# Kernel optimization log

Measured on AMD Instinct MI355X. Metric: run time of the kernel, lower is better.

## Reference

```python
import jax, jax.numpy as jnp
import numpy as np

N_NODES = 51200
N_GRAPHS = 64
NODES_PER_GRAPH = 800
N_EDGES = 819200
DIM_IN = 128
DIM_HIDDEN = 64
HEADS = 3
DIM_OUT = 64


def leaky(x, slope):
    return jnp.where(x >= 0, x, slope * x)


def setup_inputs() -> dict:
    key = jax.random.key(0)
    ks = jax.random.split(key, 12)
    s = lambda fan_in: 1.0 / np.sqrt(fan_in)
    X = jax.random.normal(ks[0], (N_NODES, DIM_IN), dtype=jnp.float32)
    edge_indices = jax.random.randint(ks[1], (2, N_EDGES), 0, N_NODES, dtype=jnp.int32)
    ptr = (jnp.arange(N_GRAPHS + 1, dtype=jnp.int32) * NODES_PER_GRAPH)
    # linearSeq: Linear(dim_in, dim_hidden) + LeakyReLU
    W1 = jax.random.uniform(ks[2], (DIM_IN, DIM_HIDDEN), jnp.float32, -s(DIM_IN), s(DIM_IN))
    b1 = jax.random.uniform(ks[3], (DIM_HIDDEN,), jnp.float32, -s(DIM_IN), s(DIM_IN))
    # GATConv params: lin_src/lin_dst (no bias), att_src/att_dst, bias (concat=False -> out_channels)
    W_src = jax.random.uniform(ks[4], (DIM_HIDDEN, HEADS * DIM_HIDDEN), jnp.float32, -s(DIM_HIDDEN), s(DIM_HIDDEN))
    W_dst = jax.random.uniform(ks[5], (DIM_HIDDEN, HEADS * DIM_HIDDEN), jnp.float32, -s(DIM_HIDDEN), s(DIM_HIDDEN))
    att_src = jax.random.normal(ks[6], (HEADS, DIM_HIDDEN), dtype=jnp.float32) * 0.1
    att_dst = jax.random.normal(ks[7], (HEADS, DIM_HIDDEN), dtype=jnp.float32) * 0.1
    gat_bias = jnp.zeros((DIM_HIDDEN,), dtype=jnp.float32)
    # linear_final: Linear(2*dim_hidden, dim_out)
    Wf = jax.random.uniform(ks[8], (2 * DIM_HIDDEN, DIM_OUT), jnp.float32, -s(2 * DIM_HIDDEN), s(2 * DIM_HIDDEN))
    bf = jax.random.uniform(ks[9], (DIM_OUT,), jnp.float32, -s(2 * DIM_HIDDEN), s(2 * DIM_HIDDEN))
    return {"X": X, "W1": W1, "b1": b1, "W_src": W_src, "W_dst": W_dst,
            "att_src": att_src, "att_dst": att_dst, "gat_bias": gat_bias,
            "Wf": Wf, "bf": bf, "edge_indices": edge_indices, "ptr": ptr}


def reference(X, W1, b1, W_src, W_dst, att_src, att_dst, gat_bias, Wf, bf, edge_indices, ptr):
    N = X.shape[0]
    src, dst = edge_indices[0], edge_indices[1]  # message flows src -> dst
    # input projection
    h = leaky(X @ W1 + b1, 0.01)                                  # [N, DH]
    # GATConv (heads=3, concat=False, add_self_loops=False)
    x_src = (h @ W_src).reshape(N, HEADS, DIM_HIDDEN)             # [N, H, C]
    x_dst = (h @ W_dst).reshape(N, HEADS, DIM_HIDDEN)
    a_src = jnp.einsum('nhc,hc->nh', x_src, att_src)              # [N, H]
    a_dst = jnp.einsum('nhc,hc->nh', x_dst, att_dst)
    logits = leaky(a_src[src] + a_dst[dst], 0.2)                  # [E, H]
    # segment softmax over incoming edges of each target node
    m = jax.ops.segment_max(logits, dst, num_segments=N)          # [N, H]
    e = jnp.exp(logits - m[dst])
    denom = jax.ops.segment_sum(e, dst, num_segments=N)           # [N, H]
    attn = e / denom[dst]                                         # [E, H]
    msg = x_src[src] * attn[..., None]                            # [E, H, C]
    agg = jax.ops.segment_sum(msg, dst, num_segments=N)           # [N, H, C]
    out = agg.mean(axis=1) + gat_bias                             # concat=False -> head mean
    # final head
    cat = jnp.concatenate([h, out], axis=1)                       # [N, 2*DH]
    y = leaky(cat, 0.01) @ Wf + bf                                # [N, DO]
    # aggregate_using_ptr: mean-pool nodes per graph using CSR ptr
    node_graph = jnp.searchsorted(ptr, jnp.arange(N), side='right') - 1
    sums = jax.ops.segment_sum(y, node_graph, num_segments=ptr.shape[0] - 1)
    counts = (ptr[1:] - ptr[:-1]).astype(y.dtype)
    pooled = sums / counts[:, None]                               # [n_graphs, DO]
    return pooled, attn
```

## Files before the change

### kernel.cpp

```cpp
#include <hip/hip_runtime.h>
#include <hip/hip_bf16.h>

#define N_NODES   51200
#define N_GRAPHS  64
#define N_EDGES   819200
#define DIM_IN    128
#define DH        64
#define HEADS     3
#define DIM_OUT   64
#define CAP       96
#define NPART     8
#define PART_SZ   (N_NODES / NPART)

typedef __hip_bfloat16 bf16;
typedef short bf16x8 __attribute__((ext_vector_type(8)));
typedef float f32x4  __attribute__((ext_vector_type(4)));
typedef float f32x2  __attribute__((ext_vector_type(2)));

__device__ __forceinline__ float b2f(bf16 x) { return __bfloat162float(x); }
__device__ __forceinline__ bf16  f2b(float x) { return __float2bfloat16(x); }
__device__ __forceinline__ short f2bs(float x) { return (short)__bfloat16_as_ushort(f2b(x)); }
__device__ __forceinline__ float leaky(float x, float s) { return x >= 0.f ? x : s * x; }
__device__ __forceinline__ float ldin(const void* p, size_t i, int f32) {
    return f32 ? ((const float*)p)[i] : b2f(((const bf16*)p)[i]);
}
__device__ __forceinline__ bf16x8 ld8(const void* p, size_t i, int f32) {
    if (!f32) return *((const bf16x8*)((const short*)p + i));
    const float* f = (const float*)p + i;
    bf16x8 r;
    #pragma unroll
    for (int j = 0; j < 8; ++j) r[j] = f2bs(f[j]);
    return r;
}

__global__ __launch_bounds__(256) void detect_kernel(const unsigned short* __restrict__ Xu,
                                                     int* __restrict__ flag) {
    __shared__ int cnt;
    int tid = threadIdx.x;
    if (tid == 0) cnt = 0;
    __syncthreads();
    int local = 0;
    for (int i = tid * 2; i < 8192; i += 512) {
        unsigned e = (Xu[i] >> 7) & 0xFF;
        if (e >= 110 && e <= 135) local++;
    }
    atomicAdd(&cnt, local);
    __syncthreads();
    if (tid == 0) *flag = (cnt < 2048) ? 1 : 0;
}

__global__ __launch_bounds__(256) void scatter_prep_kernel(const int* __restrict__ src,
                                                           const int* __restrict__ dst,
                                                           int* __restrict__ cursor,
                                                           unsigned short* __restrict__ bucket,
                                                           const void* __restrict__ W1,
                                                           const void* __restrict__ Wsrc,
                                                           const void* __restrict__ Wdst,
                                                           const void* __restrict__ Wf,
                                                           const void* __restrict__ att_src,
                                                           const void* __restrict__ att_dst,
                                                           const int* __restrict__ flagp,
                                                           short* __restrict__ W1t,
                                                           short* __restrict__ Wallt,
                                                           short* __restrict__ Wft,
                                                           short* __restrict__ Wat) {
    if (blockIdx.x < NPART * (N_EDGES / 2048)) {
        const int p = blockIdx.x & (NPART - 1);
        const int slice = blockIdx.x >> 3;
        const int lo = p * PART_SZ, hi = lo + PART_SZ;
        const int base = slice * 2048 + threadIdx.x;
        #pragma unroll
        for (int t = 0; t < 8; ++t) {
            int e = base + t * 256;
            int d = dst[e];
            if (d >= lo && d < hi) {
                int pos = atomicAdd(&cursor[d], 1);
                if (pos < CAP) bucket[(size_t)d * CAP + pos] = (unsigned short)src[e];
            }
        }
        return;
    }
    const int f32 = *flagp;
    int idx = (blockIdx.x - NPART * (N_EDGES / 2048)) * 256 + threadIdx.x;
    if (idx < 8192) {
        int n = idx >> 7, k = idx & 127;
        W1t[idx] = f2bs(ldin(W1, (size_t)k * 64 + n, f32));
    } else if (idx < 8192 + 12288) {
        int j = idx - 8192;
        int n = j >> 6, k = j & 63;
        Wallt[j] = f2bs(ldin(Wsrc, (size_t)k * 192 + n, f32));
    } else if (idx < 8192 + 12288 + 8192) {
        int j = idx - 20480;
        int n = j >> 7, k = j & 127;
        Wft[j] = f2bs(ldin(Wf, (size_t)k * 64 + n, f32));
    } else if (idx < 8192 + 12288 + 8192 + 1024) {
        int j = idx - 28672;
        int n = j >> 6, k = j & 63;
        float v = 0.f;
        if (n < 3) {
            for (int c = 0; c < 64; ++c)
                v += ldin(Wsrc, (size_t)k * 192 + n * 64 + c, f32) * ldin(att_src, n * 64 + c, f32);
        } else if (n < 6) {
            for (int c = 0; c < 64; ++c)
                v += ldin(Wdst, (size_t)k * 192 + (n - 3) * 64 + c, f32) * ldin(att_dst, (n - 3) * 64 + c, f32);
        }
        Wat[j] = f2bs(v);
    }
}

__global__ __launch_bounds__(256) void k1_kernel(const void* __restrict__ X,
                                                 const short* __restrict__ W1t,
                                                 const short* __restrict__ Wallt,
                                                 const short* __restrict__ Wat,
                                                 const void* __restrict__ b1,
                                                 const int* __restrict__ flagp,
                                                 bf16* __restrict__ h_bf,
                                                 unsigned* __restrict__ x8,
                                                 float* __restrict__ a_src4,
                                                 float* __restrict__ a_dst4) {
    const int f32 = *flagp;
    __shared__ short hs[64 * 72];
    const int tid  = threadIdx.x;
    const int w    = tid >> 6;
    const int lane = tid & 63;
    const int lm   = lane & 15;
    const int q    = lane >> 4;
    const int row0 = blockIdx.x * 64;

    const float bias = ldin(b1, w * 16 + lm, f32);
    for (int mt = 0; mt < 4; ++mt) {
        f32x4 acc = {0.f, 0.f, 0.f, 0.f};
        #pragma unroll
        for (int kc = 0; kc < 4; ++kc) {
            bf16x8 a = ld8(X, (size_t)(row0 + mt * 16 + lm) * 128 + kc * 32 + q * 8, f32);
            bf16x8 b = *((const bf16x8*)(W1t + (size_t)(w * 16 + lm) * 128 + kc * 32 + q * 8));
            acc = __builtin_amdgcn_mfma_f32_16x16x32_bf16(a, b, acc, 0, 0, 0);
        }
        #pragma unroll
        for (int r = 0; r < 4; ++r) {
            int row = mt * 16 + q * 4 + r;
            float v = leaky(acc[r] + bias, 0.01f);
            short hv = f2bs(v);
            hs[row * 72 + w * 16 + lm] = hv;
            h_bf[(size_t)(row0 + row) * 64 + w * 16 + lm] = __ushort_as_bfloat16((unsigned short)hv);
        }
    }
    __syncthreads();

    for (int mt = 0; mt < 4; ++mt) {
        bf16x8 a0 = *((const bf16x8*)(hs + (mt * 16 + lm) * 72 + q * 8));
        bf16x8 a1 = *((const bf16x8*)(hs + (mt * 16 + lm) * 72 + 32 + q * 8));
        f32x4 acc[3];
        #pragma unroll
        for (int hh = 0; hh < 3; ++hh) {
            acc[hh] = (f32x4){0.f, 0.f, 0.f, 0.f};
            bf16x8 b0 = *((const bf16x8*)(Wallt + (size_t)(hh * 64 + w * 16 + lm) * 64 + q * 8));
            bf16x8 b1v = *((const bf16x8*)(Wallt + (size_t)(hh * 64 + w * 16 + lm) * 64 + 32 + q * 8));
            acc[hh] = __builtin_amdgcn_mfma_f32_16x16x32_bf16(a0, b0, acc[hh], 0, 0, 0);
            acc[hh] = __builtin_amdgcn_mfma_f32_16x16x32_bf16(a1, b1v, acc[hh], 0, 0, 0);
        }
        #pragma unroll
        for (int r = 0; r < 4; ++r) {
            int row = row0 + mt * 16 + q * 4 + r;
            unsigned p = (unsigned)__builtin_amdgcn_cvt_pk_fp8_f32(acc[0][r], acc[1][r], 0, false);
            p = (unsigned)__builtin_amdgcn_cvt_pk_fp8_f32(acc[2][r], 0.f, (int)p, true);
            x8[(size_t)row * 64 + w * 16 + lm] = p;
        }
        if (w == mt) {
            f32x4 acca = {0.f, 0.f, 0.f, 0.f};
            bf16x8 b0 = *((const bf16x8*)(Wat + (size_t)lm * 64 + q * 8));
            bf16x8 b1v = *((const bf16x8*)(Wat + (size_t)lm * 64 + 32 + q * 8));
            acca = __builtin_amdgcn_mfma_f32_16x16x32_bf16(a0, b0, acca, 0, 0, 0);
            acca = __builtin_amdgcn_mfma_f32_16x16x32_bf16(a1, b1v, acca, 0, 0, 0);
            if (lm < 6) {
                #pragma unroll
                for (int r = 0; r < 4; ++r) {
                    int row = row0 + mt * 16 + q * 4 + r;
                    if (lm < 3) a_src4[(size_t)row * 4 + lm] = acca[r];
                    else        a_dst4[(size_t)row * 4 + (lm - 3)] = acca[r];
                }
            }
        }
    }
}

__global__ __launch_bounds__(256) void edge_kernel(const unsigned short* __restrict__ bucket,
                                                   const int* __restrict__ cursor,
                                                   const float* __restrict__ a_src4,
                                                   const float* __restrict__ a_dst4,
                                                   const unsigned* __restrict__ x8,
                                                   const void* __restrict__ gat_bias,
                                                   const int* __restrict__ flagp,
                                                   float4* __restrict__ dstinfo,
                                                   bf16* __restrict__ out_agg) {
    const int f32 = *flagp;
    const int lane = threadIdx.x & 63;
    const int w = threadIdx.x >> 6;
    const int n = blockIdx.x * 4 + w;
    const int dg = min(cursor[n], CAP);
    const float4 ad = ((const float4*)a_dst4)[n];
    __shared__ float4 buf[4][64];
    float den0 = 0.f, den1 = 0.f, den2 = 0.f;
    float acc0 = 0.f, acc1 = 0.f, acc2 = 0.f;
    for (int c0 = 0; c0 < dg; c0 += 64) {
        int cnt = min(64, dg - c0);
        if (lane < cnt) {
            int s = bucket[(size_t)n * CAP + c0 + lane];
            const float4 as = ((const float4*)a_src4)[s];
            float e0 = __expf(leaky(as.x + ad.x, 0.2f));
            float e1 = __expf(leaky(as.y + ad.y, 0.2f));
            float e2 = __expf(leaky(as.z + ad.z, 0.2f));
            buf[w][lane] = make_float4(e0, e1, e2, __int_as_float(s));
        }
        asm volatile("s_waitcnt lgkmcnt(0)" ::: "memory");
        int j = 0;
        for (; j + 8 <= cnt; j += 8) {
            float4 r[8]; int xv[8];
            #pragma unroll
            for (int u = 0; u < 8; ++u) r[u] = buf[w][j + u];
            #pragma unroll
            for (int u = 0; u < 8; ++u)
                xv[u] = (int)x8[(size_t)__float_as_int(r[u].w) * 64 + lane];
            #pragma unroll
            for (int u = 0; u < 8; ++u) {
                f32x2 p = __builtin_amdgcn_cvt_pk_f32_fp8(xv[u], false);
                acc0 += r[u].x * p[0];
                acc1 += r[u].y * p[1];
                acc2 += r[u].z * __builtin_amdgcn_cvt_f32_fp8(xv[u], 2);
                den0 += r[u].x; den1 += r[u].y; den2 += r[u].z;
            }
        }
        for (; j < cnt; ++j) {
            float4 r = buf[w][j];
            int xv = (int)x8[(size_t)__float_as_int(r.w) * 64 + lane];
            f32x2 p = __builtin_amdgcn_cvt_pk_f32_fp8(xv, false);
            acc0 += r.x * p[0];
            acc1 += r.y * p[1];
            acc2 += r.z * __builtin_amdgcn_cvt_f32_fp8(xv, 2);
            den0 += r.x; den1 += r.y; den2 += r.z;
        }
    }
    float inv0 = den0 > 0.f ? 1.f / den0 : 0.f;
    float inv1 = den1 > 0.f ? 1.f / den1 : 0.f;
    float inv2 = den2 > 0.f ? 1.f / den2 : 0.f;
    float outv = (acc0 * inv0 + acc1 * inv1 + acc2 * inv2) * (1.f / 3.f) + ldin(gat_bias, lane, f32);
    out_agg[(size_t)n * DH + lane] = f2b(outv);
    if (lane == 0) {
        dstinfo[(size_t)n * 2 + 0] = make_float4(ad.x, ad.y, ad.z, 0.f);
        dstinfo[(size_t)n * 2 + 1] = make_float4(inv0, inv1, inv2, 0.f);
    }
}

__global__ __launch_bounds__(256) void attn_g3_kernel(const int* __restrict__ src,
                                                      const int* __restrict__ dst,
                                                      const float* __restrict__ a_src4,
                                                      const float4* __restrict__ dstinfo,
                                                      const bf16* __restrict__ h_bf,
                                                      const bf16* __restrict__ out_agg,
                                                      const short* __restrict__ Wft,
                                                      const void* __restrict__ bfv,
                                                      const int* __restrict__ flagp,
                                                      bf16* __restrict__ y_bf,
                                                      void* __restrict__ d_out) {
    const int f32 = *flagp;
    __shared__ short cs[64 * 136];
    if (blockIdx.x < N_EDGES / 256) {
        int e = blockIdx.x * 256 + threadIdx.x;
        int s = src[e], d = dst[e];
        const float4 as = ((const float4*)a_src4)[s];
        const float4 ad = dstinfo[(size_t)d * 2 + 0];
        const float4 cv = dstinfo[(size_t)d * 2 + 1];
        float a0 = __expf(leaky(as.x + ad.x, 0.2f)) * cv.x;
        float a1 = __expf(leaky(as.y + ad.y, 0.2f)) * cv.y;
        float a2 = __expf(leaky(as.z + ad.z, 0.2f)) * cv.z;
        size_t o = (size_t)N_GRAPHS * DIM_OUT + (size_t)e * 3;
        if (f32) {
            float* p = (float*)d_out;
            p[o] = a0; p[o + 1] = a1; p[o + 2] = a2;
        } else {
            bf16* p = (bf16*)d_out;
            p[o] = f2b(a0); p[o + 1] = f2b(a1); p[o + 2] = f2b(a2);
        }
        return;
    }
    const int bid  = blockIdx.x - N_EDGES / 256;
    const int tid  = threadIdx.x;
    const int w    = tid >> 6;
    const int lane = tid & 63;
    const int lm   = lane & 15;
    const int q    = lane >> 4;
    const int row0 = bid * 64;
    for (int idx = tid; idx < 64 * 64; idx += 256) {
        int r = idx >> 6, k = idx & 63;
        cs[r * 136 + k] = f2bs(leaky(b2f(h_bf[(size_t)(row0 + r) * 64 + k]), 0.01f));
    }
    for (int idx = tid; idx < 64 * 64; idx += 256) {
        int r = idx >> 6, k = idx & 63;
        cs[r * 136 + 64 + k] = f2bs(leaky(b2f(out_agg[(size_t)(row0 + r) * 64 + k]), 0.01f));
    }
    __syncthreads();
    const float bias = ldin(bfv, w * 16 + lm, f32);
    for (int mt = 0; mt < 4; ++mt) {
        f32x4 acc = {0.f, 0.f, 0.f, 0.f};
        #pragma unroll
        for (int kc = 0; kc < 4; ++kc) {
            bf16x8 a = *((const bf16x8*)(cs + (mt * 16 + lm) * 136 + kc * 32 + q * 8));
            bf16x8 b = *((const bf16x8*)(Wft + (size_t)(w * 16 + lm) * 128 + kc * 32 + q * 8));
            acc = __builtin_amdgcn_mfma_f32_16x16x32_bf16(a, b, acc, 0, 0, 0);
        }
        #pragma unroll
        for (int r = 0; r < 4; ++r) {
            int row = row0 + mt * 16 + q * 4 + r;
            y_bf[(size_t)row * 64 + w * 16 + lm] = f2b(acc[r] + bias);
        }
    }
}

__global__ __launch_bounds__(1024) void pool_kernel(const bf16* __restrict__ y_bf,
                                                    const int* __restrict__ ptr,
                                                    const int* __restrict__ flagp,
                                                    void* __restrict__ d_out) {
    __shared__ float part[16][64];
    const int f32 = *flagp;
    const int g = blockIdx.x;
    const int w = threadIdx.x >> 6, lane = threadIdx.x & 63;
    const int lo = ptr[g], hi = ptr[g + 1];
    const int cnt = hi - lo;
    float s = 0.f;
    for (int i = lo + w; i < hi; i += 16) s += b2f(y_bf[(size_t)i * DIM_OUT + lane]);
    part[w][lane] = s;
    __syncthreads();
    if (threadIdx.x < 64) {
        float t = 0.f;
        #pragma unroll
        for (int k = 0; k < 16; ++k) t += part[k][threadIdx.x];
        float v = t / (float)cnt;
        if (f32) ((float*)d_out)[g * DIM_OUT + threadIdx.x] = v;
        else     ((bf16*)d_out)[g * DIM_OUT + threadIdx.x]  = f2b(v);
    }
}

extern "C" void kernel_launch(void* const* d_in, const int* in_sizes, int n_in,
                              void* d_out, int out_size, void* d_ws, size_t ws_size,
                              hipStream_t stream) {
    const void* X        = d_in[0];
    const void* W1       = d_in[1];
    const void* b1       = d_in[2];
    const void* Wsrc     = d_in[3];
    const void* Wdst     = d_in[4];
    const void* att_src  = d_in[5];
    const void* att_dst  = d_in[6];
    const void* gat_bias = d_in[7];
    const void* Wf       = d_in[8];
    const void* bfv      = d_in[9];
    const int*  ei       = (const int*)d_in[10];
    const int*  ptr      = (const int*)d_in[11];
    const int*  src  = ei;
    const int*  dstp = ei + N_EDGES;

    char* ws = (char*)d_ws;
    size_t off_b = 0;
    auto alloc = [&](size_t bytes) -> char* {
        char* p = ws + off_b;
        off_b += (bytes + 255) & ~(size_t)255;
        return p;
    };
    int*     flag    = (int*)    alloc(256);
    short*   W1t     = (short*)  alloc(8192 * 2);
    short*   Wallt   = (short*)  alloc(12288 * 2);
    short*   Wft     = (short*)  alloc(8192 * 2);
    short*   Wat     = (short*)  alloc(1024 * 2);
    bf16*    h_bf    = (bf16*)   alloc((size_t)N_NODES * 64 * 2);
    unsigned* x8     = (unsigned*)alloc((size_t)N_NODES * 64 * 4);
    float*   a_src4  = (float*)  alloc((size_t)N_NODES * 16);
    float*   a_dst4  = (float*)  alloc((size_t)N_NODES * 16);
    float4*  dstinfo = (float4*) alloc((size_t)N_NODES * 2 * 16);
    bf16*    out_agg = (bf16*)   alloc((size_t)N_NODES * 64 * 2);
    int*     cursor  = (int*)    alloc((size_t)N_NODES * 4);
    unsigned short* bucket = (unsigned short*)alloc((size_t)N_NODES * CAP * 2);
    bf16*    y_bf    = (bf16*)   x8;
    if (off_b > ws_size) return;

    hipLaunchKernelGGL(detect_kernel, dim3(1), dim3(256), 0, stream,
                       (const unsigned short*)X, flag);
    hipMemsetAsync(cursor, 0, (size_t)N_NODES * 4, stream);
    hipLaunchKernelGGL(scatter_prep_kernel,
                       dim3(NPART * (N_EDGES / 2048) + 116), dim3(256), 0, stream,
                       src, dstp, cursor, bucket,
                       W1, Wsrc, Wdst, Wf, att_src, att_dst, flag, W1t, Wallt, Wft, Wat);
    hipLaunchKernelGGL(k1_kernel, dim3(N_NODES / 64), dim3(256), 0, stream,
                       X, W1t, Wallt, Wat, b1, flag, h_bf, x8, a_src4, a_dst4);
    hipLaunchKernelGGL(edge_kernel, dim3(N_NODES / 4), dim3(256), 0, stream,
                       bucket, cursor, a_src4, a_dst4, x8, gat_bias, flag, dstinfo, out_agg);
    hipLaunchKernelGGL(attn_g3_kernel, dim3(N_EDGES / 256 + N_NODES / 64), dim3(256), 0, stream,
                       src, dstp, a_src4, dstinfo, h_bf, out_agg, Wft, bfv, flag, y_bf, d_out);
    hipLaunchKernelGGL(pool_kernel, dim3(N_GRAPHS), dim3(1024), 0, stream, y_bf, ptr, flag, d_out);
}
```

Baseline: 239.6 us.

## Aggregate h before W_src projection and apply projection after aggregation

```diff
diff --git a/kernel.cpp b/kernel.cpp
--- a/kernel.cpp
+++ b/kernel.cpp
@@ -15,7 +15,6 @@
 typedef __hip_bfloat16 bf16;
 typedef short bf16x8 __attribute__((ext_vector_type(8)));
 typedef float f32x4  __attribute__((ext_vector_type(4)));
-typedef float f32x2  __attribute__((ext_vector_type(2)));
 
 __device__ __forceinline__ float b2f(bf16 x) { return __bfloat162float(x); }
 __device__ __forceinline__ bf16  f2b(float x) { return __float2bfloat16(x); }
@@ -61,7 +60,7 @@
                                                            const void* __restrict__ att_dst,
                                                            const int* __restrict__ flagp,
                                                            short* __restrict__ W1t,
-                                                           short* __restrict__ Wallt,
+                                                           short* __restrict__ Wspt,
                                                            short* __restrict__ Wft,
                                                            short* __restrict__ Wat) {
     if (blockIdx.x < NPART * (N_EDGES / 2048)) {
@@ -85,15 +84,17 @@
     if (idx < 8192) {
         int n = idx >> 7, k = idx & 127;
         W1t[idx] = f2bs(ldin(W1, (size_t)k * 64 + n, f32));
-    } else if (idx < 8192 + 12288) {
+    } else if (idx < 20480) {
         int j = idx - 8192;
-        int n = j >> 6, k = j & 63;
-        Wallt[j] = f2bs(ldin(Wsrc, (size_t)k * 192 + n, f32));
-    } else if (idx < 8192 + 12288 + 8192) {
+        int col = j / 192;
+        int rem = j - col * 192;
+        int h = rem >> 6, kk = rem & 63;
+        Wspt[j] = f2bs(ldin(Wsrc, (size_t)kk * 192 + h * 64 + col, f32) * (1.0f / 3.0f));
+    } else if (idx < 28672) {
         int j = idx - 20480;
         int n = j >> 7, k = j & 127;
         Wft[j] = f2bs(ldin(Wf, (size_t)k * 64 + n, f32));
-    } else if (idx < 8192 + 12288 + 8192 + 1024) {
+    } else if (idx < 29696) {
         int j = idx - 28672;
         int n = j >> 6, k = j & 63;
         float v = 0.f;
@@ -110,12 +111,10 @@
 
 __global__ __launch_bounds__(256) void k1_kernel(const void* __restrict__ X,
                                                  const short* __restrict__ W1t,
-                                                 const short* __restrict__ Wallt,
                                                  const short* __restrict__ Wat,
                                                  const void* __restrict__ b1,
                                                  const int* __restrict__ flagp,
                                                  bf16* __restrict__ h_bf,
-                                                 unsigned* __restrict__ x8,
                                                  float* __restrict__ a_src4,
                                                  float* __restrict__ a_dst4) {
     const int f32 = *flagp;
@@ -147,38 +146,21 @@
     }
     __syncthreads();
 
-    for (int mt = 0; mt < 4; ++mt) {
-        bf16x8 a0 = *((const bf16x8*)(hs + (mt * 16 + lm) * 72 + q * 8));
-        bf16x8 a1 = *((const bf16x8*)(hs + (mt * 16 + lm) * 72 + 32 + q * 8));
-        f32x4 acc[3];
-        #pragma unroll
-        for (int hh = 0; hh < 3; ++hh) {
-            acc[hh] = (f32x4){0.f, 0.f, 0.f, 0.f};
-            bf16x8 b0 = *((const bf16x8*)(Wallt + (size_t)(hh * 64 + w * 16 + lm) * 64 + q * 8));
-            bf16x8 b1v = *((const bf16x8*)(Wallt + (size_t)(hh * 64 + w * 16 + lm) * 64 + 32 + q * 8));
-            acc[hh] = __builtin_amdgcn_mfma_f32_16x16x32_bf16(a0, b0, acc[hh], 0, 0, 0);
-            acc[hh] = __builtin_amdgcn_mfma_f32_16x16x32_bf16(a1, b1v, acc[hh], 0, 0, 0);
-        }
-        #pragma unroll
-        for (int r = 0; r < 4; ++r) {
-            int row = row0 + mt * 16 + q * 4 + r;
-            unsigned p = (unsigned)__builtin_amdgcn_cvt_pk_fp8_f32(acc[0][r], acc[1][r], 0, false);
-            p = (unsigned)__builtin_amdgcn_cvt_pk_fp8_f32(acc[2][r], 0.f, (int)p, true);
-            x8[(size_t)row * 64 + w * 16 + lm] = p;
-        }
-        if (w == mt) {
-            f32x4 acca = {0.f, 0.f, 0.f, 0.f};
-            bf16x8 b0 = *((const bf16x8*)(Wat + (size_t)lm * 64 + q * 8));
-            bf16x8 b1v = *((const bf16x8*)(Wat + (size_t)lm * 64 + 32 + q * 8));
-            acca = __builtin_amdgcn_mfma_f32_16x16x32_bf16(a0, b0, acca, 0, 0, 0);
-            acca = __builtin_amdgcn_mfma_f32_16x16x32_bf16(a1, b1v, acca, 0, 0, 0);
-            if (lm < 6) {
-                #pragma unroll
-                for (int r = 0; r < 4; ++r) {
-                    int row = row0 + mt * 16 + q * 4 + r;
-                    if (lm < 3) a_src4[(size_t)row * 4 + lm] = acca[r];
-                    else        a_dst4[(size_t)row * 4 + (lm - 3)] = acca[r];
-                }
+    {
+        const int mt = w;
+        bf16x8 a0  = *((const bf16x8*)(hs + (mt * 16 + lm) * 72 + q * 8));
+        bf16x8 a1  = *((const bf16x8*)(hs + (mt * 16 + lm) * 72 + 32 + q * 8));
+        bf16x8 b0  = *((const bf16x8*)(Wat + (size_t)lm * 64 + q * 8));
+        bf16x8 b1v = *((const bf16x8*)(Wat + (size_t)lm * 64 + 32 + q * 8));
+        f32x4 acca = {0.f, 0.f, 0.f, 0.f};
+        acca = __builtin_amdgcn_mfma_f32_16x16x32_bf16(a0, b0, acca, 0, 0, 0);
+        acca = __builtin_amdgcn_mfma_f32_16x16x32_bf16(a1, b1v, acca, 0, 0, 0);
+        if (lm < 6) {
+            #pragma unroll
+            for (int r = 0; r < 4; ++r) {
+                int row = row0 + mt * 16 + q * 4 + r;
+                if (lm < 3) a_src4[(size_t)row * 4 + lm] = acca[r];
+                else        a_dst4[(size_t)row * 4 + (lm - 3)] = acca[r];
             }
         }
     }
@@ -188,12 +170,9 @@
                                                    const int* __restrict__ cursor,
                                                    const float* __restrict__ a_src4,
                                                    const float* __restrict__ a_dst4,
-                                                   const unsigned* __restrict__ x8,
-                                                   const void* __restrict__ gat_bias,
-                                                   const int* __restrict__ flagp,
+                                                   const unsigned short* __restrict__ hu,
                                                    float4* __restrict__ dstinfo,
-                                                   bf16* __restrict__ out_agg) {
-    const int f32 = *flagp;
+                                                   bf16* __restrict__ wagg) {
     const int lane = threadIdx.x & 63;
     const int w = threadIdx.x >> 6;
     const int n = blockIdx.x * 4 + w;
@@ -205,7 +184,7 @@
     for (int c0 = 0; c0 < dg; c0 += 64) {
         int cnt = min(64, dg - c0);
         if (lane < cnt) {
-            int s = bucket[(size_t)n * CAP + c0 + lane];
+            int s = bucket[n * CAP + c0 + lane];
             const float4 as = ((const float4*)a_src4)[s];
             float e0 = __expf(leaky(as.x + ad.x, 0.2f));
             float e1 = __expf(leaky(as.y + ad.y, 0.2f));
@@ -215,36 +194,34 @@
         asm volatile("s_waitcnt lgkmcnt(0)" ::: "memory");
         int j = 0;
         for (; j + 8 <= cnt; j += 8) {
-            float4 r[8]; int xv[8];
+            float4 r[8]; unsigned short hv[8];
             #pragma unroll
             for (int u = 0; u < 8; ++u) r[u] = buf[w][j + u];
             #pragma unroll
             for (int u = 0; u < 8; ++u)
-                xv[u] = (int)x8[(size_t)__float_as_int(r[u].w) * 64 + lane];
+                hv[u] = hu[(((unsigned)__float_as_int(r[u].w)) << 6) | (unsigned)lane];
             #pragma unroll
             for (int u = 0; u < 8; ++u) {
-                f32x2 p = __builtin_amdgcn_cvt_pk_f32_fp8(xv[u], false);
-                acc0 += r[u].x * p[0];
-                acc1 += r[u].y * p[1];
-                acc2 += r[u].z * __builtin_amdgcn_cvt_f32_fp8(xv[u], 2);
-                den0 += r[u].x; den1 += r[u].y; den2 += r[u].z;
+                float f = b2f(__ushort_as_bfloat16(hv[u]));
+                acc0 += r[u].x * f; acc1 += r[u].y * f; acc2 += r[u].z * f;
+                den0 += r[u].x;     den1 += r[u].y;     den2 += r[u].z;
             }
         }
         for (; j < cnt; ++j) {
             float4 r = buf[w][j];
-            int xv = (int)x8[(size_t)__float_as_int(r.w) * 64 + lane];
-            f32x2 p = __builtin_amdgcn_cvt_pk_f32_fp8(xv, false);
-            acc0 += r.x * p[0];
-            acc1 += r.y * p[1];
-            acc2 += r.z * __builtin_amdgcn_cvt_f32_fp8(xv, 2);
-            den0 += r.x; den1 += r.y; den2 += r.z;
+            unsigned short hvv = hu[(((unsigned)__float_as_int(r.w)) << 6) | (unsigned)lane];
+            float f = b2f(__ushort_as_bfloat16(hvv));
+            acc0 += r.x * f; acc1 += r.y * f; acc2 += r.z * f;
+            den0 += r.x;     den1 += r.y;     den2 += r.z;
         }
     }
     float inv0 = den0 > 0.f ? 1.f / den0 : 0.f;
     float inv1 = den1 > 0.f ? 1.f / den1 : 0.f;
     float inv2 = den2 > 0.f ? 1.f / den2 : 0.f;
-    float outv = (acc0 * inv0 + acc1 * inv1 + acc2 * inv2) * (1.f / 3.f) + ldin(gat_bias, lane, f32);
-    out_agg[(size_t)n * DH + lane] = f2b(outv);
+    size_t wb = (size_t)n * 192;
+    wagg[wb + lane]       = f2b(acc0 * inv0);
+    wagg[wb + 64 + lane]  = f2b(acc1 * inv1);
+    wagg[wb + 128 + lane] = f2b(acc2 * inv2);
     if (lane == 0) {
         dstinfo[(size_t)n * 2 + 0] = make_float4(ad.x, ad.y, ad.z, 0.f);
         dstinfo[(size_t)n * 2 + 1] = make_float4(inv0, inv1, inv2, 0.f);
@@ -256,8 +233,10 @@
                                                       const float* __restrict__ a_src4,
                                                       const float4* __restrict__ dstinfo,
                                                       const bf16* __restrict__ h_bf,
-                                                      const bf16* __restrict__ out_agg,
+                                                      const bf16* __restrict__ wagg,
+                                                      const short* __restrict__ Wspt,
                                                       const short* __restrict__ Wft,
+                                                      const void* __restrict__ gat_bias,
                                                       const void* __restrict__ bfv,
                                                       const int* __restrict__ flagp,
                                                       bf16* __restrict__ y_bf,
@@ -294,9 +273,23 @@
         int r = idx >> 6, k = idx & 63;
         cs[r * 136 + k] = f2bs(leaky(b2f(h_bf[(size_t)(row0 + r) * 64 + k]), 0.01f));
     }
-    for (int idx = tid; idx < 64 * 64; idx += 256) {
-        int r = idx >> 6, k = idx & 63;
-        cs[r * 136 + 64 + k] = f2bs(leaky(b2f(out_agg[(size_t)(row0 + r) * 64 + k]), 0.01f));
+    {
+        const int col = w * 16 + lm;
+        const float gb = ldin(gat_bias, col, f32);
+        for (int mt = 0; mt < 4; ++mt) {
+            f32x4 acc = {0.f, 0.f, 0.f, 0.f};
+            #pragma unroll
+            for (int kc = 0; kc < 6; ++kc) {
+                bf16x8 a = *((const bf16x8*)((const short*)wagg + (size_t)(row0 + mt * 16 + lm) * 192 + kc * 32 + q * 8));
+                bf16x8 b = *((const bf16x8*)(Wspt + (size_t)col * 192 + kc * 32 + q * 8));
+                acc = __builtin_amdgcn_mfma_f32_16x16x32_bf16(a, b, acc, 0, 0, 0);
+            }
+            #pragma unroll
+            for (int r = 0; r < 4; ++r) {
+                int row = mt * 16 + q * 4 + r;
+                cs[row * 136 + 64 + col] = f2bs(leaky(acc[r] + gb, 0.01f));
+            }
+        }
     }
     __syncthreads();
     const float bias = ldin(bfv, w * 16 + lm, f32);
@@ -367,18 +360,17 @@
     };
     int*     flag    = (int*)    alloc(256);
     short*   W1t     = (short*)  alloc(8192 * 2);
-    short*   Wallt   = (short*)  alloc(12288 * 2);
+    short*   Wspt    = (short*)  alloc(12288 * 2);
     short*   Wft     = (short*)  alloc(8192 * 2);
     short*   Wat     = (short*)  alloc(1024 * 2);
     bf16*    h_bf    = (bf16*)   alloc((size_t)N_NODES * 64 * 2);
-    unsigned* x8     = (unsigned*)alloc((size_t)N_NODES * 64 * 4);
     float*   a_src4  = (float*)  alloc((size_t)N_NODES * 16);
     float*   a_dst4  = (float*)  alloc((size_t)N_NODES * 16);
     float4*  dstinfo = (float4*) alloc((size_t)N_NODES * 2 * 16);
-    bf16*    out_agg = (bf16*)   alloc((size_t)N_NODES * 64 * 2);
+    bf16*    wagg    = (bf16*)   alloc((size_t)N_NODES * 192 * 2);
     int*     cursor  = (int*)    alloc((size_t)N_NODES * 4);
     unsigned short* bucket = (unsigned short*)alloc((size_t)N_NODES * CAP * 2);
-    bf16*    y_bf    = (bf16*)   x8;
+    bf16*    y_bf    = (bf16*)   bucket;
     if (off_b > ws_size) return;
 
     hipLaunchKernelGGL(detect_kernel, dim3(1), dim3(256), 0, stream,
@@ -387,12 +379,14 @@
     hipLaunchKernelGGL(scatter_prep_kernel,
                        dim3(NPART * (N_EDGES / 2048) + 116), dim3(256), 0, stream,
                        src, dstp, cursor, bucket,
-                       W1, Wsrc, Wdst, Wf, att_src, att_dst, flag, W1t, Wallt, Wft, Wat);
+                       W1, Wsrc, Wdst, Wf, att_src, att_dst, flag, W1t, Wspt, Wft, Wat);
     hipLaunchKernelGGL(k1_kernel, dim3(N_NODES / 64), dim3(256), 0, stream,
-                       X, W1t, Wallt, Wat, b1, flag, h_bf, x8, a_src4, a_dst4);
+                       X, W1t, Wat, b1, flag, h_bf, a_src4, a_dst4);
     hipLaunchKernelGGL(edge_kernel, dim3(N_NODES / 4), dim3(256), 0, stream,
-                       bucket, cursor, a_src4, a_dst4, x8, gat_bias, flag, dstinfo, out_agg);
+                       bucket, cursor, a_src4, a_dst4,
+                       (const unsigned short*)h_bf, dstinfo, wagg);
     hipLaunchKernelGGL(attn_g3_kernel, dim3(N_EDGES / 256 + N_NODES / 64), dim3(256), 0, stream,
-                       src, dstp, a_src4, dstinfo, h_bf, out_agg, Wft, bfv, flag, y_bf, d_out);
+                       src, dstp, a_src4, dstinfo, h_bf, wagg, Wspt, Wft,
+                       gat_bias, bfv, flag, y_bf, d_out);
     hipLaunchKernelGGL(pool_kernel, dim3(N_GRAPHS), dim3(1024), 0, stream, y_bf, ptr, flag, d_out);
 }
```

Result: no change. 237.5 us (-0.9%).
